# Performance work log

Hardware: AMD Instinct MI355X
Metric: run time of the kernel (lower is better)

Reference implementation:

```python
import jax, jax.numpy as jnp
import numpy as np

EPS = 1e-15

def _artanh(x):
    return jnp.arctanh(jnp.clip(x, -1 + 1e-7, 1 - 1e-7))

def mobius_matvec(M, x, c=1.0):
    # Poincare ball Mobius matrix-vector product (geoopt convention), c=1.
    sqc = jnp.sqrt(c)
    xn = jnp.maximum(jnp.linalg.norm(x, axis=-1, keepdims=True), EPS)
    mx = x @ M.T
    mxn = jnp.maximum(jnp.linalg.norm(mx, axis=-1, keepdims=True), EPS)
    return jnp.tanh(mxn / xn * _artanh(sqc * xn)) * mx / (mxn * sqc)

def mobius_add(x, y, c=1.0):
    x2 = jnp.sum(x * x, axis=-1, keepdims=True)
    y2 = jnp.sum(y * y, axis=-1, keepdims=True)
    xy = jnp.sum(x * y, axis=-1, keepdims=True)
    num = (1 + 2 * c * xy + c * y2) * x + (1 - c * x2) * y
    den = 1 + 2 * c * xy + (c ** 2) * x2 * y2
    return num / (den + EPS)

def hyp_linear(x, W, b):
    return mobius_add(mobius_matvec(W, x), b)

def hyperbolic_scores(q, k):
    # q,k: [B,H,S,D], elementwise clamp_max as in source
    q = jnp.minimum(q, 1 - 1e-5)
    k = jnp.minimum(k, 1 - 1e-5)
    q2 = jnp.sum(q * q, axis=-1, keepdims=True)          # [B,H,S,1]
    k2 = jnp.sum(k * k, axis=-1, keepdims=True)          # [B,H,S,1]
    qk = jnp.einsum('bhqd,bhkd->bhqk', q, k)             # [B,H,S,S]
    numer = 2 * (q2 + jnp.swapaxes(k2, -2, -1) - 2 * qk)
    denom = (1 - q2) * jnp.swapaxes(1 - k2, -2, -1) + EPS
    dist_sq = jnp.arccosh(jnp.maximum(1 + numer / denom, 1.0))
    dist_sq = jnp.maximum(dist_sq, 1e-7)
    return -dist_sq

def reference(x, Wq, bq, Wk, bk, Wv, bv, Wo, bo, head_scaling):
    B, S, E = x.shape
    H = head_scaling.shape[0]
    D = E // H
    q = hyp_linear(x, Wq, bq).reshape(B, S, H, D).transpose(0, 2, 1, 3)
    k = hyp_linear(x, Wk, bk).reshape(B, S, H, D).transpose(0, 2, 1, 3)
    v = hyp_linear(x, Wv, bv).reshape(B, S, H, D).transpose(0, 2, 1, 3)
    scores = hyperbolic_scores(q, k) / (head_scaling * (D ** 0.5))  # [B,H,S,S]
    w = jax.nn.softmax(scores, axis=-1)
    out = jnp.einsum('bhqk,bhkd->bhqd', w, v)
    out = out.transpose(0, 2, 1, 3).reshape(B, S, E)
    return hyp_linear(out, Wo, bo)

def setup_inputs() -> dict:
    key = jax.random.key(0)
    ks = jax.random.split(key, 6)
    B, S, E, H = 8, 1024, 768, 12
    x = jax.random.normal(ks[0], (B, S, E), dtype=jnp.float32) * 0.05
    Wq = jax.random.normal(ks[1], (E, E), dtype=jnp.float32) * 0.05
    Wk = jax.random.normal(ks[2], (E, E), dtype=jnp.float32) * 0.05
    Wv = jax.random.normal(ks[3], (E, E), dtype=jnp.float32) * 0.05
    Wo = jax.random.normal(ks[4], (E, E), dtype=jnp.float32) * 0.05
    z = jnp.zeros((E,), dtype=jnp.float32)
    return {'x': x, 'Wq': Wq, 'bq': z, 'Wk': Wk, 'bk': z, 'Wv': Wv, 'bv': z,
            'Wo': Wo, 'bo': z, 'head_scaling': jnp.ones((H, 1, 1), dtype=jnp.float32)}
```

## Files before the change

kernel.cpp:

```cpp
#include <hip/hip_runtime.h>
#include <hip/hip_bf16.h>
#include <math.h>

#define Bb 8
#define Ss 1024
#define Ee 768
#define Hh 12
#define Dd 64
#define Mm (Bb*Ss)
#define NW (Ee*Ee)
#define LQKV 2304

typedef short  s16x8 __attribute__((ext_vector_type(8)));
typedef float  f32x4 __attribute__((ext_vector_type(4)));

__device__ __forceinline__ unsigned short f2bf(float f) {
    __hip_bfloat16 b = __float2bfloat16(f);
    return *reinterpret_cast<unsigned short*>(&b);
}
__device__ __forceinline__ float bf2f(unsigned short h) {
    return __uint_as_float(((unsigned)h) << 16);
}

__device__ __forceinline__ float block_sum_256(float v, float* red) {
    #pragma unroll
    for (int off = 32; off > 0; off >>= 1) v += __shfl_down(v, off, 64);
    __syncthreads();
    if ((threadIdx.x & 63) == 0) red[threadIdx.x >> 6] = v;
    __syncthreads();
    return red[0] + red[1] + red[2] + red[3];
}

__global__ __launch_bounds__(256) void pack_x_kernel(const float* __restrict__ A,
                                                     unsigned short* __restrict__ Ab,
                                                     float* __restrict__ xn) {
    __shared__ float red[4];
    size_t row = blockIdx.x;
    const float* a = A + row * Ee;
    float ssum = 0.f;
    #pragma unroll
    for (int l = 0; l < 3; ++l) {
        float x = a[threadIdx.x + l*256];
        ssum += x*x;
        Ab[row*Ee + threadIdx.x + l*256] = f2bf(x);
    }
    float tot = block_sum_256(ssum, red);
    if (threadIdx.x == 0) xn[row] = fmaxf(sqrtf(tot), 1e-15f);
}

__global__ __launch_bounds__(256) void row_norm_bf16(const unsigned short* __restrict__ A,
                                                     float* __restrict__ out) {
    __shared__ float red[4];
    size_t row = blockIdx.x;
    const unsigned short* a = A + row * LQKV;
    float s = 0.f;
    #pragma unroll
    for (int l = 0; l < 3; ++l) { float x = bf2f(a[threadIdx.x + l*256]); s += x*x; }
    float tot = block_sum_256(s, red);
    if (threadIdx.x == 0) out[row] = fmaxf(sqrtf(tot), 1e-15f);
}

__global__ __launch_bounds__(256) void pack_w_kernel(const float* __restrict__ W0,
                                                     const float* __restrict__ W1,
                                                     const float* __restrict__ W2,
                                                     const float* __restrict__ W3,
                                                     unsigned short* __restrict__ Wb) {
    const float* src = (blockIdx.y == 0) ? W0 : (blockIdx.y == 1) ? W1
                     : (blockIdx.y == 2) ? W2 : W3;
    size_t idx = (size_t)blockIdx.x * 1024 + threadIdx.x * 4;
    float4 v = *reinterpret_cast<const float4*>(&src[idx]);
    uint2 o;
    o.x = (unsigned)f2bf(v.x) | ((unsigned)f2bf(v.y) << 16);
    o.y = (unsigned)f2bf(v.z) | ((unsigned)f2bf(v.w) << 16);
    *reinterpret_cast<uint2*>(Wb + (size_t)blockIdx.y * NW + idx) = o;
}

template<int OUT16>
__global__ __launch_bounds__(256) void gemm_bf16_nt(const unsigned short* __restrict__ A,
                                                    int lda,
                                                    const unsigned short* __restrict__ B,
                                                    void* __restrict__ Cout, int ldc) {
    __shared__ alignas(16) unsigned short As[64][64];
    __shared__ alignas(16) unsigned short Bs[128][64];
    const int tid = threadIdx.x, lane = tid & 63, w = tid >> 6;
    const int g = lane >> 4, lg = lane & 15;
    const int mBase = blockIdx.x * 64, nBase = blockIdx.y * 128;
    const int wr = w >> 1, wc = w & 1;
    f32x4 zero4 = {0.f,0.f,0.f,0.f};
    f32x4 acc[2][4];
    #pragma unroll
    for (int i = 0; i < 2; ++i)
        #pragma unroll
        for (int j = 0; j < 4; ++j) acc[i][j] = zero4;

    for (int k0 = 0; k0 < Ee; k0 += 64) {
        s16x8 av[2], bv[4];
        #pragma unroll
        for (int i = 0; i < 2; ++i) {
            int s = tid + i*256, r = s >> 3, c = s & 7;
            av[i] = *(const s16x8*)&A[(size_t)(mBase + r)*lda + k0 + c*8];
        }
        #pragma unroll
        for (int i = 0; i < 4; ++i) {
            int s = tid + i*256, r = s >> 3, c = s & 7;
            bv[i] = *(const s16x8*)&B[(size_t)(nBase + r)*Ee + k0 + c*8];
        }
        __syncthreads();
        #pragma unroll
        for (int i = 0; i < 2; ++i) {
            int s = tid + i*256, r = s >> 3, c = s & 7;
            *(s16x8*)&As[r][((c ^ (r & 7)))*8] = av[i];
        }
        #pragma unroll
        for (int i = 0; i < 4; ++i) {
            int s = tid + i*256, r = s >> 3, c = s & 7;
            *(s16x8*)&Bs[r][((c ^ (r & 7)))*8] = bv[i];
        }
        __syncthreads();
        #pragma unroll
        for (int kk = 0; kk < 2; ++kk) {
            s16x8 af[2], bfr[4];
            #pragma unroll
            for (int mi = 0; mi < 2; ++mi) {
                int ar = wr*32 + mi*16 + lg;
                af[mi] = *(const s16x8*)&As[ar][(((kk*4 + g) ^ (ar & 7)))*8];
            }
            #pragma unroll
            for (int ni = 0; ni < 4; ++ni) {
                int br = wc*64 + ni*16 + lg;
                bfr[ni] = *(const s16x8*)&Bs[br][(((kk*4 + g) ^ (br & 7)))*8];
            }
            #pragma unroll
            for (int mi = 0; mi < 2; ++mi)
                #pragma unroll
                for (int ni = 0; ni < 4; ++ni)
                    acc[mi][ni] = __builtin_amdgcn_mfma_f32_16x16x32_bf16(af[mi], bfr[ni], acc[mi][ni], 0, 0, 0);
        }
    }
    #pragma unroll
    for (int mi = 0; mi < 2; ++mi)
        #pragma unroll
        for (int ni = 0; ni < 4; ++ni)
            #pragma unroll
            for (int r = 0; r < 4; ++r) {
                size_t off = (size_t)(mBase + wr*32 + mi*16 + g*4 + r)*ldc + nBase + wc*64 + ni*16 + lg;
                if (OUT16) ((unsigned short*)Cout)[off] = f2bf(acc[mi][ni][r]);
                else       ((float*)Cout)[off] = acc[mi][ni][r];
            }
}

__global__ __launch_bounds__(256) void fix_qkv_kernel(unsigned short* __restrict__ QKV,
                                                      const float* __restrict__ xn_buf,
                                                      const float* __restrict__ bq,
                                                      const float* __restrict__ bk,
                                                      const float* __restrict__ bv_,
                                                      float* __restrict__ q2g,
                                                      float* __restrict__ k2g) {
    __shared__ float red[4], red2[4];
    const int which = blockIdx.y;
    size_t row = blockIdx.x;
    const int tid = threadIdx.x;
    const float* bias = (which == 0) ? bq : (which == 1) ? bk : bv_;
    unsigned short* m = QKV + row * LQKV + which * Ee;
    float mv[3], bv[3];
    float ss = 0.f;
    #pragma unroll
    for (int l = 0; l < 3; ++l) { mv[l] = bf2f(m[tid + l*256]); ss += mv[l]*mv[l]; }
    float mxn2 = block_sum_256(ss, red);
    float mxn = fmaxf(sqrtf(mxn2), 1e-15f);
    float xn = xn_buf[row];
    float xc = fminf(xn, 1.f - 1e-7f);
    float at = 0.5f * logf((1.f + xc) / (1.f - xc));
    float th = tanhf(mxn / xn * at);
    float scale = th / mxn;
    float m2 = th * th;
    float mb = 0.f, b2 = 0.f;
    #pragma unroll
    for (int l = 0; l < 3; ++l) {
        bv[l] = bias[tid + l*256];
        mv[l] *= scale;
        mb += mv[l]*bv[l];
        b2 += bv[l]*bv[l];
    }
    mb = block_sum_256(mb, red);
    b2 = block_sum_256(b2, red2);
    float ncoef = 1.f + 2.f*mb + b2;
    float bcoef = 1.f - m2;
    float inv = 1.f / (1.f + 2.f*mb + m2*b2 + 1e-15f);
    const int lane = tid & 63, wv = tid >> 6;
    if (which < 2) {
        float* sumg = (which == 0) ? q2g : k2g;
        #pragma unroll
        for (int l = 0; l < 3; ++l) {
            float f = (ncoef*mv[l] + bcoef*bv[l]) * inv;
            float c = fminf(f, 1.f - 1e-5f);
            m[tid + l*256] = f2bf(c);
            float s2 = c*c;
            #pragma unroll
            for (int off = 1; off < 64; off <<= 1) s2 += __shfl_xor(s2, off);
            if (lane == 0) sumg[(size_t)(wv + 4*l)*Mm + row] = s2;
        }
    } else {
        #pragma unroll
        for (int l = 0; l < 3; ++l)
            m[tid + l*256] = f2bf((ncoef*mv[l] + bcoef*bv[l]) * inv);
    }
}

__global__ __launch_bounds__(256) void transpose_v_kernel(const unsigned short* __restrict__ QKV,
                                                          unsigned short* __restrict__ Vb) {
    __shared__ unsigned short t[64][72];
    const int tid = threadIdx.x;
    const int st = blockIdx.x, h = blockIdx.y, b = blockIdx.z;
    {
        int sr = tid >> 2, d0 = (tid & 3) * 16;
        const unsigned short* vp = QKV + ((size_t)b*Ss + st*64 + sr)*LQKV + 2*Ee + h*64 + d0;
        *(s16x8*)&t[sr][d0]     = *(const s16x8*)&vp[0];
        *(s16x8*)&t[sr][d0 + 8] = *(const s16x8*)&vp[8];
    }
    __syncthreads();
    {
        int d = tid >> 2, s0 = (tid & 3) * 16;
        unsigned hu[8];
        #pragma unroll
        for (int i = 0; i < 8; ++i)
            hu[i] = (unsigned)t[s0 + 2*i][d] | ((unsigned)t[s0 + 2*i + 1][d] << 16);
        size_t obase = (((size_t)b*Hh + h)*64 + d)*Ss + st*64 + s0;
        *reinterpret_cast<uint4*>(&Vb[obase])     = make_uint4(hu[0],hu[1],hu[2],hu[3]);
        *reinterpret_cast<uint4*>(&Vb[obase + 8]) = make_uint4(hu[4],hu[5],hu[6],hu[7]);
    }
}

__global__ __launch_bounds__(256) void attn_mfma2(
    unsigned short* __restrict__ QKV, const unsigned short* __restrict__ Vb,
    const float* __restrict__ q2g, const float* __restrict__ k2g,
    const float* __restrict__ hs)
{
    __shared__ alignas(16) unsigned short KHs[64][64];
    __shared__ alignas(16) unsigned short VHs[64][64];
    __shared__ alignas(16) unsigned short PHs[4][16][64];
    __shared__ float us[64], vs[64];

    const int tid = threadIdx.x, lane = tid & 63, w = tid >> 6;
    const int g = lane >> 4, lg = lane & 15;
    const int qt = blockIdx.x, h = blockIdx.y, b = blockIdx.z;
    const int q0 = qt * 64, hoff = h * 64;
    const size_t rowB = (size_t)b * Ss;

    const unsigned short* qp = QKV + (rowB + q0 + 16*w + lg)*LQKV + hoff;
    s16x8 qh[2];
    qh[0] = *(const s16x8*)&qp[g*8];
    qh[1] = *(const s16x8*)&qp[32 + g*8];
    const float nia = -1.f / (hs[h] * 8.f);
    const float q2v   = q2g[(size_t)h*Mm + rowB + q0 + 16*w + lg];
    const float a2    = 2.f * q2v;
    const float iomq2 = __builtin_amdgcn_rcpf(1.f - q2v);
    const size_t vBase = (((size_t)b*Hh + h)*64)*Ss;

    f32x4 zero4 = {0.f,0.f,0.f,0.f};
    f32x4 oacc[4];
    #pragma unroll
    for (int i = 0; i < 4; ++i) oacc[i] = zero4;
    float lsum = 0.f;

    for (int kt = 0; kt < 16; ++kt) {
        __syncthreads();
        #pragma unroll
        for (int i = 0; i < 2; ++i) {
            int s = tid + i*256, r = s >> 3, c = s & 7, cs = c ^ (r & 7);
            *(s16x8*)&KHs[r][cs*8] = *(const s16x8*)&QKV[(rowB + kt*64 + r)*LQKV + Ee + hoff + c*8];
            *(s16x8*)&VHs[r][cs*8] = *(const s16x8*)&Vb[vBase + (size_t)r*Ss + kt*64 + c*8];
        }
        if (tid < 64) {
            float k2 = k2g[(size_t)h*Mm + rowB + kt*64 + tid];
            float ik = __builtin_amdgcn_rcpf(1.f - k2);
            us[tid] = ik;
            vs[tid] = 2.f * k2 * ik;
        }
        __syncthreads();

        f32x4 sacc[4];
        #pragma unroll
        for (int i = 0; i < 4; ++i) sacc[i] = zero4;
        #pragma unroll
        for (int nt = 0; nt < 4; ++nt) {
            const int krow = nt*16 + lg, sw = krow & 7;
            #pragma unroll
            for (int dh = 0; dh < 2; ++dh) {
                s16x8 kh = *(const s16x8*)&KHs[krow][((dh*4 + g) ^ sw)*8];
                sacc[nt] = __builtin_amdgcn_mfma_f32_16x16x32_bf16(kh, qh[dh], sacc[nt], 0, 0, 0);
            }
        }

        #pragma unroll
        for (int nt = 0; nt < 4; ++nt) {
            const int j0 = nt*16 + g*4;
            float4 uq = *reinterpret_cast<const float4*>(&us[j0]);
            float4 vq = *reinterpret_cast<const float4*>(&vs[j0]);
            float uqa[4] = {uq.x, uq.y, uq.z, uq.w};
            float vqa[4] = {vq.x, vq.y, vq.z, vq.w};
            float pr[4];
            #pragma unroll
            for (int r = 0; r < 4; ++r) {
                float s  = sacc[nt][r];
                float wv_ = fmaf(-4.f, s, a2);
                float t  = fmaxf(iomq2 * fmaf(uqa[r], wv_, vqa[r]), 0.f);
                float sq = __builtin_amdgcn_sqrtf(fmaf(t, t, 2.f*t));
                float uu = t + 1.f + sq;
                float p  = __builtin_amdgcn_exp2f(nia * __builtin_amdgcn_logf(uu));
                lsum += p;
                pr[r] = p;
            }
            const int chq = ((j0 >> 3) ^ (lg & 7))*8 + (j0 & 7);
            unsigned plo = (unsigned)f2bf(pr[0]) | ((unsigned)f2bf(pr[1]) << 16);
            unsigned phi = (unsigned)f2bf(pr[2]) | ((unsigned)f2bf(pr[3]) << 16);
            *reinterpret_cast<uint2*>(&PHs[w][lg][chq]) = make_uint2(plo, phi);
        }

        #pragma unroll
        for (int jh = 0; jh < 2; ++jh) {
            s16x8 pa = *(const s16x8*)&PHs[w][lg][((jh*4 + g) ^ (lg & 7))*8];
            #pragma unroll
            for (int nt2 = 0; nt2 < 4; ++nt2) {
                const int vrow = nt2*16 + lg;
                s16x8 vh = *(const s16x8*)&VHs[vrow][((jh*4 + g) ^ (vrow & 7))*8];
                oacc[nt2] = __builtin_amdgcn_mfma_f32_16x16x32_bf16(pa, vh, oacc[nt2], 0, 0, 0);
            }
        }
    }

    lsum += __shfl_xor(lsum, 16);
    lsum += __shfl_xor(lsum, 32);
    #pragma unroll
    for (int r = 0; r < 4; ++r) {
        float lr = __shfl(lsum, g*4 + r, 64);
        float li = 1.f / lr;
        #pragma unroll
        for (int nt2 = 0; nt2 < 4; ++nt2)
            QKV[(rowB + q0 + 16*w + g*4 + r)*LQKV + 2*Ee + hoff + nt2*16 + lg] = f2bf(oacc[nt2][r] * li);
    }
}

__global__ __launch_bounds__(256) void mobius_fix_kernel(const float* __restrict__ src, float* __restrict__ dst,
                                                         const float* __restrict__ xn_buf,
                                                         const float* __restrict__ bias) {
    __shared__ float red[4], red2[4];
    size_t row = blockIdx.x;
    const float* m = src + row * Ee;
    float mv[3], bv[3];
    float ss = 0.f;
    #pragma unroll
    for (int l = 0; l < 3; ++l) { mv[l] = m[threadIdx.x + l*256]; ss += mv[l]*mv[l]; }
    float mxn2 = block_sum_256(ss, red);
    float mxn = fmaxf(sqrtf(mxn2), 1e-15f);
    float xn = xn_buf[row];
    float xc = fminf(xn, 1.f - 1e-7f);
    float at = 0.5f * logf((1.f + xc) / (1.f - xc));
    float th = tanhf(mxn / xn * at);
    float scale = th / mxn;
    float m2 = th * th;
    float mb = 0.f, b2 = 0.f;
    #pragma unroll
    for (int l = 0; l < 3; ++l) {
        bv[l] = bias[threadIdx.x + l*256];
        mv[l] *= scale;
        mb += mv[l]*bv[l];
        b2 += bv[l]*bv[l];
    }
    mb = block_sum_256(mb, red);
    b2 = block_sum_256(b2, red2);
    float ncoef = 1.f + 2.f*mb + b2;
    float bcoef = 1.f - m2;
    float inv = 1.f / (1.f + 2.f*mb + m2*b2 + 1e-15f);
    float* d = dst + row * Ee;
    #pragma unroll
    for (int l = 0; l < 3; ++l)
        d[threadIdx.x + l*256] = (ncoef*mv[l] + bcoef*bv[l]) * inv;
}

extern "C" void kernel_launch(void* const* d_in, const int* in_sizes, int n_in,
                              void* d_out, int out_size, void* d_ws, size_t ws_size,
                              hipStream_t stream) {
    const float* x  = (const float*)d_in[0];
    const float* Wq = (const float*)d_in[1];
    const float* bq = (const float*)d_in[2];
    const float* Wk = (const float*)d_in[3];
    const float* bk = (const float*)d_in[4];
    const float* Wv = (const float*)d_in[5];
    const float* bv = (const float*)d_in[6];
    const float* Wo = (const float*)d_in[7];
    const float* bo = (const float*)d_in[8];
    const float* hs = (const float*)d_in[9];
    float* out = (float*)d_out;

    const size_t NE = (size_t)Mm * Ee;
    float* ws   = (float*)d_ws;
    float* xn_x = ws;
    float* xn_o = xn_x + Mm;
    float* q2g  = xn_o + Mm;
    float* k2g  = q2g + (size_t)Hh*Mm;
    unsigned short* qkvbf = (unsigned short*)(k2g + (size_t)Hh*Mm);
    unsigned short* vtbf  = qkvbf + (size_t)Mm * LQKV;
    unsigned short* xbf   = vtbf + NE;
    unsigned short* wbf   = xbf + NE;
    float* fbuf = (float*)vtbf;

    pack_x_kernel<<<Mm, 256, 0, stream>>>(x, xbf, xn_x);
    pack_w_kernel<<<dim3(NW/1024, 4), 256, 0, stream>>>(Wq, Wk, Wv, Wo, wbf);

    gemm_bf16_nt<1><<<dim3(Mm/64, LQKV/128), 256, 0, stream>>>(xbf, Ee, wbf, qkvbf, LQKV);
    fix_qkv_kernel<<<dim3(Mm, 3), 256, 0, stream>>>(qkvbf, xn_x, bq, bk, bv, q2g, k2g);
    transpose_v_kernel<<<dim3(Ss/64, Hh, Bb), 256, 0, stream>>>(qkvbf, vtbf);

    attn_mfma2<<<dim3(Ss/64, Hh, Bb), 256, 0, stream>>>(qkvbf, vtbf, q2g, k2g, hs);

    row_norm_bf16<<<Mm, 256, 0, stream>>>(qkvbf + 2*Ee, xn_o);
    gemm_bf16_nt<0><<<dim3(Mm/64, Ee/128), 256, 0, stream>>>(qkvbf + 2*Ee, LQKV, wbf + 3*(size_t)NW, fbuf, Ee);
    mobius_fix_kernel<<<Mm, 256, 0, stream>>>(fbuf, out, xn_o, bo);
}
```

Baseline: 209.0 us.

## Software-pipeline GEMM and attention loads, fuse pack kernels and output norm

The GEMM now prefetches the next K tile into registers while the current tile is computed, with lighter barriers and raised wave priority around the MFMA sections. The attention kernel double-buffers its K/V tiles in shared memory, prefetches two tiles ahead, and reads precomputed per-row q/k scalars that fix_qkv writes. It also computes per-head squared norms of the output in its epilogue, so the separate row-norm kernel is removed. The x and W pack kernels are merged into a single launch. These changes cut launch count and hide load latency, at the cost of more registers and shared memory, which may lower occupancy.

After: 205.6 us. Within noise of the previous version (-1.6%).

```diff
diff --git a/kernel.cpp b/kernel.cpp
--- a/kernel.cpp
+++ b/kernel.cpp
@@ -6,13 +6,17 @@
 #define Ss 1024
 #define Ee 768
 #define Hh 12
-#define Dd 64
 #define Mm (Bb*Ss)
 #define NW (Ee*Ee)
 #define LQKV 2304
 
 typedef short  s16x8 __attribute__((ext_vector_type(8)));
 typedef float  f32x4 __attribute__((ext_vector_type(4)));
+
+#define FENCE() __builtin_amdgcn_sched_barrier(0)
+#define BAR_ONLY() do { FENCE(); __builtin_amdgcn_s_barrier(); FENCE(); } while(0)
+#define BAR_LGKM() do { FENCE(); asm volatile("s_waitcnt lgkmcnt(0)" ::: "memory"); FENCE(); \
+                        __builtin_amdgcn_s_barrier(); FENCE(); } while(0)
 
 __device__ __forceinline__ unsigned short f2bf(float f) {
     __hip_bfloat16 b = __float2bfloat16(f);
@@ -31,48 +35,38 @@
     return red[0] + red[1] + red[2] + red[3];
 }
 
-__global__ __launch_bounds__(256) void pack_x_kernel(const float* __restrict__ A,
-                                                     unsigned short* __restrict__ Ab,
-                                                     float* __restrict__ xn) {
+__global__ __launch_bounds__(256) void pack_xw_kernel(const float* __restrict__ x,
+    const float* __restrict__ W0, const float* __restrict__ W1,
+    const float* __restrict__ W2, const float* __restrict__ W3,
+    unsigned short* __restrict__ Xb, float* __restrict__ xn,
+    unsigned short* __restrict__ Wb) {
     __shared__ float red[4];
-    size_t row = blockIdx.x;
-    const float* a = A + row * Ee;
-    float ssum = 0.f;
-    #pragma unroll
-    for (int l = 0; l < 3; ++l) {
-        float x = a[threadIdx.x + l*256];
-        ssum += x*x;
-        Ab[row*Ee + threadIdx.x + l*256] = f2bf(x);
-    }
-    float tot = block_sum_256(ssum, red);
-    if (threadIdx.x == 0) xn[row] = fmaxf(sqrtf(tot), 1e-15f);
-}
-
-__global__ __launch_bounds__(256) void row_norm_bf16(const unsigned short* __restrict__ A,
-                                                     float* __restrict__ out) {
-    __shared__ float red[4];
-    size_t row = blockIdx.x;
-    const unsigned short* a = A + row * LQKV;
-    float s = 0.f;
-    #pragma unroll
-    for (int l = 0; l < 3; ++l) { float x = bf2f(a[threadIdx.x + l*256]); s += x*x; }
-    float tot = block_sum_256(s, red);
-    if (threadIdx.x == 0) out[row] = fmaxf(sqrtf(tot), 1e-15f);
-}
-
-__global__ __launch_bounds__(256) void pack_w_kernel(const float* __restrict__ W0,
-                                                     const float* __restrict__ W1,
-                                                     const float* __restrict__ W2,
-                                                     const float* __restrict__ W3,
-                                                     unsigned short* __restrict__ Wb) {
-    const float* src = (blockIdx.y == 0) ? W0 : (blockIdx.y == 1) ? W1
-                     : (blockIdx.y == 2) ? W2 : W3;
-    size_t idx = (size_t)blockIdx.x * 1024 + threadIdx.x * 4;
-    float4 v = *reinterpret_cast<const float4*>(&src[idx]);
-    uint2 o;
-    o.x = (unsigned)f2bf(v.x) | ((unsigned)f2bf(v.y) << 16);
-    o.y = (unsigned)f2bf(v.z) | ((unsigned)f2bf(v.w) << 16);
-    *reinterpret_cast<uint2*>(Wb + (size_t)blockIdx.y * NW + idx) = o;
+    const int bid = blockIdx.x;
+    if (bid < Mm) {
+        size_t row = bid;
+        const float* a = x + row * Ee;
+        float ssum = 0.f;
+        #pragma unroll
+        for (int l = 0; l < 3; ++l) {
+            float v = a[threadIdx.x + l*256];
+            ssum += v*v;
+            Xb[row*Ee + threadIdx.x + l*256] = f2bf(v);
+        }
+        float tot = block_sum_256(ssum, red);
+        if (threadIdx.x == 0) xn[row] = fmaxf(sqrtf(tot), 1e-15f);
+    } else {
+        int idx = bid - Mm;
+        const int perW = NW/1024;
+        int which = idx / perW;
+        int chunk = idx - which*perW;
+        const float* src = (which == 0) ? W0 : (which == 1) ? W1 : (which == 2) ? W2 : W3;
+        size_t off = (size_t)chunk * 1024 + threadIdx.x * 4;
+        float4 v = *reinterpret_cast<const float4*>(&src[off]);
+        uint2 o;
+        o.x = (unsigned)f2bf(v.x) | ((unsigned)f2bf(v.y) << 16);
+        o.y = (unsigned)f2bf(v.z) | ((unsigned)f2bf(v.w) << 16);
+        *reinterpret_cast<uint2*>(Wb + (size_t)which * NW + off) = o;
+    }
 }
 
 template<int OUT16>
@@ -86,6 +80,8 @@
     const int g = lane >> 4, lg = lane & 15;
     const int mBase = blockIdx.x * 64, nBase = blockIdx.y * 128;
     const int wr = w >> 1, wc = w & 1;
+    const int ar_ = tid >> 3, ac_ = tid & 7;
+    const int csw_ = (ac_ ^ (ar_ & 7)) * 8;
     f32x4 zero4 = {0.f,0.f,0.f,0.f};
     f32x4 acc[2][4];
     #pragma unroll
@@ -93,30 +89,27 @@
         #pragma unroll
         for (int j = 0; j < 4; ++j) acc[i][j] = zero4;
 
+    s16x8 av0, av1, bv0, bv1, bv2, bv3;
+    #define GLOAD(k0) do { \
+        av0 = *(const s16x8*)&A[(size_t)(mBase + ar_     )*lda + (k0) + ac_*8]; \
+        av1 = *(const s16x8*)&A[(size_t)(mBase + ar_ + 32)*lda + (k0) + ac_*8]; \
+        bv0 = *(const s16x8*)&B[(size_t)(nBase + ar_     )*Ee  + (k0) + ac_*8]; \
+        bv1 = *(const s16x8*)&B[(size_t)(nBase + ar_ + 32)*Ee  + (k0) + ac_*8]; \
+        bv2 = *(const s16x8*)&B[(size_t)(nBase + ar_ + 64)*Ee  + (k0) + ac_*8]; \
+        bv3 = *(const s16x8*)&B[(size_t)(nBase + ar_ + 96)*Ee  + (k0) + ac_*8]; } while(0)
+
+    GLOAD(0);
     for (int k0 = 0; k0 < Ee; k0 += 64) {
-        s16x8 av[2], bv[4];
-        #pragma unroll
-        for (int i = 0; i < 2; ++i) {
-            int s = tid + i*256, r = s >> 3, c = s & 7;
-            av[i] = *(const s16x8*)&A[(size_t)(mBase + r)*lda + k0 + c*8];
-        }
-        #pragma unroll
-        for (int i = 0; i < 4; ++i) {
-            int s = tid + i*256, r = s >> 3, c = s & 7;
-            bv[i] = *(const s16x8*)&B[(size_t)(nBase + r)*Ee + k0 + c*8];
-        }
-        __syncthreads();
-        #pragma unroll
-        for (int i = 0; i < 2; ++i) {
-            int s = tid + i*256, r = s >> 3, c = s & 7;
-            *(s16x8*)&As[r][((c ^ (r & 7)))*8] = av[i];
-        }
-        #pragma unroll
-        for (int i = 0; i < 4; ++i) {
-            int s = tid + i*256, r = s >> 3, c = s & 7;
-            *(s16x8*)&Bs[r][((c ^ (r & 7)))*8] = bv[i];
-        }
-        __syncthreads();
+        BAR_ONLY();
+        *(s16x8*)&As[ar_     ][csw_] = av0;
+        *(s16x8*)&As[ar_ + 32][csw_] = av1;
+        *(s16x8*)&Bs[ar_     ][csw_] = bv0;
+        *(s16x8*)&Bs[ar_ + 32][csw_] = bv1;
+        *(s16x8*)&Bs[ar_ + 64][csw_] = bv2;
+        *(s16x8*)&Bs[ar_ + 96][csw_] = bv3;
+        if (k0 + 64 < Ee) GLOAD(k0 + 64);
+        BAR_LGKM();
+        __builtin_amdgcn_s_setprio(1);
         #pragma unroll
         for (int kk = 0; kk < 2; ++kk) {
             s16x8 af[2], bfr[4];
@@ -136,7 +129,9 @@
                 for (int ni = 0; ni < 4; ++ni)
                     acc[mi][ni] = __builtin_amdgcn_mfma_f32_16x16x32_bf16(af[mi], bfr[ni], acc[mi][ni], 0, 0, 0);
         }
-    }
+        __builtin_amdgcn_s_setprio(0);
+    }
+    #undef GLOAD
     #pragma unroll
     for (int mi = 0; mi < 2; ++mi)
         #pragma unroll
@@ -154,8 +149,8 @@
                                                       const float* __restrict__ bq,
                                                       const float* __restrict__ bk,
                                                       const float* __restrict__ bv_,
-                                                      float* __restrict__ q2g,
-                                                      float* __restrict__ k2g) {
+                                                      float2* __restrict__ qinfo,
+                                                      float2* __restrict__ kinfo) {
     __shared__ float red[4], red2[4];
     const int which = blockIdx.y;
     size_t row = blockIdx.x;
@@ -189,7 +184,6 @@
     float inv = 1.f / (1.f + 2.f*mb + m2*b2 + 1e-15f);
     const int lane = tid & 63, wv = tid >> 6;
     if (which < 2) {
-        float* sumg = (which == 0) ? q2g : k2g;
         #pragma unroll
         for (int l = 0; l < 3; ++l) {
             float f = (ncoef*mv[l] + bcoef*bv[l]) * inv;
@@ -198,7 +192,14 @@
             float s2 = c*c;
             #pragma unroll
             for (int off = 1; off < 64; off <<= 1) s2 += __shfl_xor(s2, off);
-            if (lane == 0) sumg[(size_t)(wv + 4*l)*Mm + row] = s2;
+            if (lane == 0) {
+                if (which == 0)
+                    qinfo[(size_t)(wv + 4*l)*Mm + row] = make_float2(2.f*s2, 1.f/(1.f - s2));
+                else {
+                    float ik = 1.f/(1.f - s2);
+                    kinfo[(size_t)(wv + 4*l)*Mm + row] = make_float2(ik, 2.f*s2*ik);
+                }
+            }
         }
     } else {
         #pragma unroll
@@ -231,103 +232,132 @@
     }
 }
 
-__global__ __launch_bounds__(256) void attn_mfma2(
+__global__ __launch_bounds__(256) void attn_mfma3(
     unsigned short* __restrict__ QKV, const unsigned short* __restrict__ Vb,
-    const float* __restrict__ q2g, const float* __restrict__ k2g,
-    const float* __restrict__ hs)
+    const float2* __restrict__ qinfo, const float2* __restrict__ kinfo,
+    const float* __restrict__ hs, float* __restrict__ osq)
 {
-    __shared__ alignas(16) unsigned short KHs[64][64];
-    __shared__ alignas(16) unsigned short VHs[64][64];
+    __shared__ alignas(16) unsigned short KHs[2][64][64];
+    __shared__ alignas(16) unsigned short VHs[2][64][64];
     __shared__ alignas(16) unsigned short PHs[4][16][64];
-    __shared__ float us[64], vs[64];
+    __shared__ float us[2][64], vs[2][64];
 
     const int tid = threadIdx.x, lane = tid & 63, w = tid >> 6;
     const int g = lane >> 4, lg = lane & 15;
     const int qt = blockIdx.x, h = blockIdx.y, b = blockIdx.z;
     const int q0 = qt * 64, hoff = h * 64;
     const size_t rowB = (size_t)b * Ss;
+    const size_t hMm = (size_t)h * Mm;
+    const size_t vBase = (((size_t)b*Hh + h)*64)*Ss;
+    const int rr = tid >> 3, cc = tid & 7;
+    const int csw = (cc ^ (rr & 7)) * 8;
+
+    const unsigned short* kgp = &QKV[(rowB + rr)*LQKV + Ee + hoff + cc*8];
+    const unsigned short* vgp = &Vb[vBase + (size_t)rr*Ss + cc*8];
 
     const unsigned short* qp = QKV + (rowB + q0 + 16*w + lg)*LQKV + hoff;
-    s16x8 qh[2];
-    qh[0] = *(const s16x8*)&qp[g*8];
-    qh[1] = *(const s16x8*)&qp[32 + g*8];
+    s16x8 qh0 = *(const s16x8*)&qp[g*8];
+    s16x8 qh1 = *(const s16x8*)&qp[32 + g*8];
+    float2 qi = qinfo[hMm + rowB + q0 + 16*w + lg];
+    const float a2 = qi.x, iomq2 = qi.y;
     const float nia = -1.f / (hs[h] * 8.f);
-    const float q2v   = q2g[(size_t)h*Mm + rowB + q0 + 16*w + lg];
-    const float a2    = 2.f * q2v;
-    const float iomq2 = __builtin_amdgcn_rcpf(1.f - q2v);
-    const size_t vBase = (((size_t)b*Hh + h)*64)*Ss;
+
+    s16x8 cka, ckb, cva, cvb, nka, nkb, nva, nvb;
+    #define LOADKV(ka,kb,va,vb_,kt) do { \
+        ka  = *(const s16x8*)&kgp[(size_t)(kt)*64*LQKV]; \
+        kb  = *(const s16x8*)&kgp[(size_t)(kt)*64*LQKV + (size_t)32*LQKV]; \
+        va  = *(const s16x8*)&vgp[(kt)*64]; \
+        vb_ = *(const s16x8*)&vgp[(size_t)32*Ss + (kt)*64]; } while(0)
+    #define WRITEKV(bi,ka,kb,va,vb_) do { \
+        *(s16x8*)&KHs[bi][rr     ][csw] = ka; \
+        *(s16x8*)&KHs[bi][rr + 32][csw] = kb; \
+        *(s16x8*)&VHs[bi][rr     ][csw] = va; \
+        *(s16x8*)&VHs[bi][rr + 32][csw] = vb_; } while(0)
+
+    LOADKV(cka,ckb,cva,cvb, 0);
+    LOADKV(nka,nkb,nva,nvb, 1);
+    float2 uvC = make_float2(0.f,0.f), uvN = make_float2(0.f,0.f);
+    if (tid < 64) uvC = kinfo[hMm + rowB + tid];
+    if (tid < 64) uvN = kinfo[hMm + rowB + 64 + tid];
+    WRITEKV(0, cka,ckb,cva,cvb);
+    if (tid < 64) { us[0][tid] = uvC.x; vs[0][tid] = uvC.y; }
+    BAR_LGKM();
 
     f32x4 zero4 = {0.f,0.f,0.f,0.f};
     f32x4 oacc[4];
     #pragma unroll
     for (int i = 0; i < 4; ++i) oacc[i] = zero4;
     float lsum = 0.f;
+    int cur = 0;
 
     for (int kt = 0; kt < 16; ++kt) {
-        __syncthreads();
-        #pragma unroll
-        for (int i = 0; i < 2; ++i) {
-            int s = tid + i*256, r = s >> 3, c = s & 7, cs = c ^ (r & 7);
-            *(s16x8*)&KHs[r][cs*8] = *(const s16x8*)&QKV[(rowB + kt*64 + r)*LQKV + Ee + hoff + c*8];
-            *(s16x8*)&VHs[r][cs*8] = *(const s16x8*)&Vb[vBase + (size_t)r*Ss + kt*64 + c*8];
-        }
-        if (tid < 64) {
-            float k2 = k2g[(size_t)h*Mm + rowB + kt*64 + tid];
-            float ik = __builtin_amdgcn_rcpf(1.f - k2);
-            us[tid] = ik;
-            vs[tid] = 2.f * k2 * ik;
-        }
-        __syncthreads();
+        if (kt < 15) {
+            WRITEKV(cur^1, nka,nkb,nva,nvb);
+            if (tid < 64) { us[cur^1][tid] = uvN.x; vs[cur^1][tid] = uvN.y; }
+        }
+        if (kt < 14) {
+            LOADKV(nka,nkb,nva,nvb, kt+2);
+            if (tid < 64) uvN = kinfo[hMm + rowB + (kt+2)*64 + tid];
+        }
 
         f32x4 sacc[4];
         #pragma unroll
         for (int i = 0; i < 4; ++i) sacc[i] = zero4;
+        __builtin_amdgcn_s_setprio(1);
         #pragma unroll
         for (int nt = 0; nt < 4; ++nt) {
             const int krow = nt*16 + lg, sw = krow & 7;
-            #pragma unroll
-            for (int dh = 0; dh < 2; ++dh) {
-                s16x8 kh = *(const s16x8*)&KHs[krow][((dh*4 + g) ^ sw)*8];
-                sacc[nt] = __builtin_amdgcn_mfma_f32_16x16x32_bf16(kh, qh[dh], sacc[nt], 0, 0, 0);
-            }
-        }
+            s16x8 kh0 = *(const s16x8*)&KHs[cur][krow][((g    ) ^ sw)*8];
+            s16x8 kh1 = *(const s16x8*)&KHs[cur][krow][((4 + g) ^ sw)*8];
+            sacc[nt] = __builtin_amdgcn_mfma_f32_16x16x32_bf16(kh0, qh0, sacc[nt], 0, 0, 0);
+            sacc[nt] = __builtin_amdgcn_mfma_f32_16x16x32_bf16(kh1, qh1, sacc[nt], 0, 0, 0);
+        }
+        __builtin_amdgcn_s_setprio(0);
 
         #pragma unroll
         for (int nt = 0; nt < 4; ++nt) {
             const int j0 = nt*16 + g*4;
-            float4 uq = *reinterpret_cast<const float4*>(&us[j0]);
-            float4 vq = *reinterpret_cast<const float4*>(&vs[j0]);
+            float4 uq = *reinterpret_cast<const float4*>(&us[cur][j0]);
+            float4 vq = *reinterpret_cast<const float4*>(&vs[cur][j0]);
             float uqa[4] = {uq.x, uq.y, uq.z, uq.w};
             float vqa[4] = {vq.x, vq.y, vq.z, vq.w};
             float pr[4];
             #pragma unroll
             for (int r = 0; r < 4; ++r) {
-                float s  = sacc[nt][r];
+                float s   = sacc[nt][r];
                 float wv_ = fmaf(-4.f, s, a2);
-                float t  = fmaxf(iomq2 * fmaf(uqa[r], wv_, vqa[r]), 0.f);
-                float sq = __builtin_amdgcn_sqrtf(fmaf(t, t, 2.f*t));
-                float uu = t + 1.f + sq;
-                float p  = __builtin_amdgcn_exp2f(nia * __builtin_amdgcn_logf(uu));
+                float t   = fmaxf(iomq2 * fmaf(uqa[r], wv_, vqa[r]), 0.f);
+                float sq  = __builtin_amdgcn_sqrtf(fmaf(t, t, t + t));
+                float uu  = t + 1.f + sq;
+                float p   = __builtin_amdgcn_exp2f(nia * __builtin_amdgcn_logf(uu));
                 lsum += p;
                 pr[r] = p;
             }
+            unsigned p01, p23;
+            asm("v_cvt_pk_bf16_f32 %0, %1, %2" : "=v"(p01) : "v"(pr[0]), "v"(pr[1]));
+            asm("v_cvt_pk_bf16_f32 %0, %1, %2" : "=v"(p23) : "v"(pr[2]), "v"(pr[3]));
             const int chq = ((j0 >> 3) ^ (lg & 7))*8 + (j0 & 7);
-            unsigned plo = (unsigned)f2bf(pr[0]) | ((unsigned)f2bf(pr[1]) << 16);
-            unsigned phi = (unsigned)f2bf(pr[2]) | ((unsigned)f2bf(pr[3]) << 16);
-            *reinterpret_cast<uint2*>(&PHs[w][lg][chq]) = make_uint2(plo, phi);
-        }
-
+            *reinterpret_cast<uint2*>(&PHs[w][lg][chq]) = make_uint2(p01, p23);
+        }
+
+        __builtin_amdgcn_s_setprio(1);
         #pragma unroll
         for (int jh = 0; jh < 2; ++jh) {
             s16x8 pa = *(const s16x8*)&PHs[w][lg][((jh*4 + g) ^ (lg & 7))*8];
             #pragma unroll
             for (int nt2 = 0; nt2 < 4; ++nt2) {
                 const int vrow = nt2*16 + lg;
-                s16x8 vh = *(const s16x8*)&VHs[vrow][((jh*4 + g) ^ (vrow & 7))*8];
+                s16x8 vh = *(const s16x8*)&VHs[cur][vrow][((jh*4 + g) ^ (vrow & 7))*8];
                 oacc[nt2] = __builtin_amdgcn_mfma_f32_16x16x32_bf16(pa, vh, oacc[nt2], 0, 0, 0);
             }
         }
-    }
+        __builtin_amdgcn_s_setprio(0);
+
+        BAR_LGKM();
+        cur ^= 1;
+    }
+    #undef LOADKV
+    #undef WRITEKV
 
     lsum += __shfl_xor(lsum, 16);
     lsum += __shfl_xor(lsum, 32);
@@ -335,15 +365,25 @@
     for (int r = 0; r < 4; ++r) {
         float lr = __shfl(lsum, g*4 + r, 64);
         float li = 1.f / lr;
-        #pragma unroll
-        for (int nt2 = 0; nt2 < 4; ++nt2)
-            QKV[(rowB + q0 + 16*w + g*4 + r)*LQKV + 2*Ee + hoff + nt2*16 + lg] = f2bf(oacc[nt2][r] * li);
-    }
-}
-
-__global__ __launch_bounds__(256) void mobius_fix_kernel(const float* __restrict__ src, float* __restrict__ dst,
-                                                         const float* __restrict__ xn_buf,
-                                                         const float* __restrict__ bias) {
+        float sq = 0.f;
+        #pragma unroll
+        for (int nt2 = 0; nt2 < 4; ++nt2) {
+            float o = oacc[nt2][r] * li;
+            sq = fmaf(o, o, sq);
+            QKV[(rowB + q0 + 16*w + g*4 + r)*LQKV + 2*Ee + hoff + nt2*16 + lg] = f2bf(o);
+        }
+        sq += __shfl_xor(sq, 1);
+        sq += __shfl_xor(sq, 2);
+        sq += __shfl_xor(sq, 4);
+        sq += __shfl_xor(sq, 8);
+        if (lg == 0) osq[hMm + rowB + q0 + 16*w + g*4 + r] = sq;
+    }
+}
+
+__global__ __launch_bounds__(256) void mobius_fix_final(const float* __restrict__ src,
+                                                        float* __restrict__ dst,
+                                                        const float* __restrict__ osq,
+                                                        const float* __restrict__ bias) {
     __shared__ float red[4], red2[4];
     size_t row = blockIdx.x;
     const float* m = src + row * Ee;
@@ -353,7 +393,10 @@
     for (int l = 0; l < 3; ++l) { mv[l] = m[threadIdx.x + l*256]; ss += mv[l]*mv[l]; }
     float mxn2 = block_sum_256(ss, red);
     float mxn = fmaxf(sqrtf(mxn2), 1e-15f);
-    float xn = xn_buf[row];
+    float ss2 = 0.f;
+    #pragma unroll
+    for (int hh = 0; hh < Hh; ++hh) ss2 += osq[(size_t)hh*Mm + row];
+    float xn = fmaxf(sqrtf(ss2), 1e-15f);
     float xc = fminf(xn, 1.f - 1e-7f);
     float at = 0.5f * logf((1.f + xc) / (1.f - xc));
     float th = tanhf(mxn / xn * at);
@@ -394,27 +437,25 @@
     float* out = (float*)d_out;
 
     const size_t NE = (size_t)Mm * Ee;
-    float* ws   = (float*)d_ws;
-    float* xn_x = ws;
-    float* xn_o = xn_x + Mm;
-    float* q2g  = xn_o + Mm;
-    float* k2g  = q2g + (size_t)Hh*Mm;
-    unsigned short* qkvbf = (unsigned short*)(k2g + (size_t)Hh*Mm);
+    float* ws    = (float*)d_ws;
+    float* xn_x  = ws;
+    float* osq   = xn_x + Mm;
+    float2* qinfo = (float2*)(osq + (size_t)Hh*Mm);
+    float2* kinfo = qinfo + (size_t)Hh*Mm;
+    unsigned short* qkvbf = (unsigned short*)(kinfo + (size_t)Hh*Mm);
     unsigned short* vtbf  = qkvbf + (size_t)Mm * LQKV;
     unsigned short* xbf   = vtbf + NE;
     unsigned short* wbf   = xbf + NE;
     float* fbuf = (float*)vtbf;
 
-    pack_x_kernel<<<Mm, 256, 0, stream>>>(x, xbf, xn_x);
-    pack_w_kernel<<<dim3(NW/1024, 4), 256, 0, stream>>>(Wq, Wk, Wv, Wo, wbf);
+    pack_xw_kernel<<<Mm + 4*(NW/1024), 256, 0, stream>>>(x, Wq, Wk, Wv, Wo, xbf, xn_x, wbf);
 
     gemm_bf16_nt<1><<<dim3(Mm/64, LQKV/128), 256, 0, stream>>>(xbf, Ee, wbf, qkvbf, LQKV);
-    fix_qkv_kernel<<<dim3(Mm, 3), 256, 0, stream>>>(qkvbf, xn_x, bq, bk, bv, q2g, k2g);
+    fix_qkv_kernel<<<dim3(Mm, 3), 256, 0, stream>>>(qkvbf, xn_x, bq, bk, bv, qinfo, kinfo);
     transpose_v_kernel<<<dim3(Ss/64, Hh, Bb), 256, 0, stream>>>(qkvbf, vtbf);
 
-    attn_mfma2<<<dim3(Ss/64, Hh, Bb), 256, 0, stream>>>(qkvbf, vtbf, q2g, k2g, hs);
-
-    row_norm_bf16<<<Mm, 256, 0, stream>>>(qkvbf + 2*Ee, xn_o);
+    attn_mfma3<<<dim3(Ss/64, Hh, Bb), 256, 0, stream>>>(qkvbf, vtbf, qinfo, kinfo, hs, osq);
+
     gemm_bf16_nt<0><<<dim3(Mm/64, Ee/128), 256, 0, stream>>>(qkvbf + 2*Ee, LQKV, wbf + 3*(size_t)NW, fbuf, Ee);
-    mobius_fix_kernel<<<Mm, 256, 0, stream>>>(fbuf, out, xn_o, bo);
-}
+    mobius_fix_final<<<Mm, 256, 0, stream>>>(fbuf, out, osq, bo);
+}
```
